# Optimization experiments

Measured on AMD Instinct MI355X. Metric: run time of the kernel, lower is better.

The kernel has to match this reference:

```python
import jax, jax.numpy as jnp
import numpy as np
import math

B, T, C, N = 2, 2048, 1024, 16  # batch, seq, h_dim, n_heads
D = C // N

def setup_inputs() -> dict:
    key = jax.random.key(0)
    k1, k2, k3 = jax.random.split(key, 3)
    x = jax.random.normal(k1, (B, T, C), dtype=jnp.float32)
    Wqkv = jax.random.normal(k2, (C, 3 * C), dtype=jnp.float32) * (1.0 / math.sqrt(C))
    bqkv = jnp.zeros((3 * C,), dtype=jnp.float32)
    Wproj = jax.random.normal(k3, (C, C), dtype=jnp.float32) * (1.0 / math.sqrt(C))
    bproj = jnp.zeros((C,), dtype=jnp.float32)
    return {"x": x, "Wqkv": Wqkv, "bqkv": bqkv, "Wproj": Wproj, "bproj": bproj}

def reference(x, Wqkv, bqkv, Wproj, bproj):
    B_, T_, C_ = x.shape
    N_, D_ = N, C_ // N
    qkv = x @ Wqkv + bqkv                                  # (B,T,3C)
    q, k, v = jnp.split(qkv, 3, axis=-1)
    q = q.reshape(B_, T_, N_, D_).transpose(0, 2, 1, 3)    # (B,N,T,D)
    k = k.reshape(B_, T_, N_, D_).transpose(0, 2, 1, 3)
    v = v.reshape(B_, T_, N_, D_).transpose(0, 2, 1, 3)
    # causal mask: lower-triangular ones, broadcast over (B, 1, T, T)
    mask = jnp.tril(jnp.ones((T_, T_), dtype=jnp.float32))[None, None]
    weights = jnp.einsum('bntd,bnsd->bnts', q, k) / math.sqrt(D_)
    # faithful to original: adds tiny 1e-9 to masked entries (NOT -inf)
    weights = weights + (1.0 - mask) * 1e-9
    normalized = jax.nn.softmax(weights, axis=-1)
    attn = jnp.einsum('bnts,bnsd->bntd', normalized, v)    # (B,N,T,D)
    attn = attn.transpose(0, 2, 1, 3).reshape(B_, T_, N_ * D_)
    out = attn @ Wproj + bproj                              # (B,T,C)
    return out
```

## Files before the change

kernel.cpp:

```cpp
#include <hip/hip_runtime.h>
#include <hip/hip_bf16.h>

#define BB 2
#define TT 2048
#define CC 1024
#define NHEAD 16
#define DHEAD 64
#define MM (BB*TT)
#define KVB 128

using bf16 = __hip_bfloat16;
typedef __bf16 bf16x8 __attribute__((ext_vector_type(8)));
typedef __bf16 bf16x4 __attribute__((ext_vector_type(4)));
typedef float f32x4 __attribute__((ext_vector_type(4)));

static __device__ __forceinline__ bf16 f2b(float f) { return __float2bfloat16(f); }
static __device__ __forceinline__ float fast_exp2(float f) { return __builtin_amdgcn_exp2f(f); }

static __device__ __forceinline__ void gload16(const bf16* g, bf16* l) {
  __builtin_amdgcn_global_load_lds((__attribute__((address_space(1))) const void*)g,
                                   (__attribute__((address_space(3))) void*)l, 16, 0, 0);
}

__global__ __launch_bounds__(256)
void k_prep(const float* __restrict__ x, bf16* __restrict__ Xb,
            const float* __restrict__ Wqkv, bf16* __restrict__ WqkvT,
            const float* __restrict__ Wproj, bf16* __restrict__ WprojT)
{
  int bid = blockIdx.x;
  const int tid = threadIdx.x;
  if (bid < 1024) {
    int base = bid * 1024 + tid;
#pragma unroll
    for (int k = 0; k < 4; ++k) {
      int i = base + k * 256;
      float4 v = reinterpret_cast<const float4*>(x)[i];
      bf16 o[4] = { f2b(v.x), f2b(v.y), f2b(v.z), f2b(v.w) };
      reinterpret_cast<uint2*>(Xb)[i] = *reinterpret_cast<uint2*>(o);
    }
    return;
  }
  bid -= 1024;
  __shared__ float tile[32][33];
  const float* W; bf16* WT; int R, Cc, bx, by;
  if (bid < 3072) {
    W = Wqkv;  WT = WqkvT;  R = CC; Cc = 3*CC;
    bx = bid % 96; by = bid / 96;
  } else {
    bid -= 3072;
    W = Wproj; WT = WprojT; R = CC; Cc = CC;
    bx = bid % 32; by = bid / 32;
  }
  int c0 = bx * 32, r0 = by * 32;
  int tx = tid & 31, ty = tid >> 5;
#pragma unroll
  for (int i = 0; i < 4; ++i)
    tile[ty + 8*i][tx] = W[(size_t)(r0 + ty + 8*i) * Cc + c0 + tx];
  __syncthreads();
#pragma unroll
  for (int i = 0; i < 4; ++i)
    WT[(size_t)(c0 + ty + 8*i) * R + r0 + tx] = f2b(tile[tx][ty + 8*i]);
}

__global__ void k_vtrans(const bf16* __restrict__ V, bf16* __restrict__ VT) {
  __shared__ bf16 tile[32][33];
  const int bn = blockIdx.z;
  const int d0 = blockIdx.x * 32, t0 = blockIdx.y * 32;
  const size_t base = (size_t)bn * TT * DHEAD;
  int tx = threadIdx.x, ty = threadIdx.y;
#pragma unroll
  for (int i = 0; i < 4; ++i)
    tile[ty + 8*i][tx] = V[base + (size_t)(t0 + ty + 8*i) * DHEAD + d0 + tx];
  __syncthreads();
#pragma unroll
  for (int i = 0; i < 4; ++i)
    VT[base + (size_t)(d0 + ty + 8*i) * TT + t0 + tx] = tile[tx][ty + 8*i];
}

#define NTK 32
__global__ __launch_bounds__(512, 2)
void k_gemm_qkv(const bf16* __restrict__ Ag, const bf16* __restrict__ Bg,
                const float* __restrict__ bias,
                bf16* __restrict__ Qb, bf16* __restrict__ Kb, bf16* __restrict__ Vb)
{
  const int tid = threadIdx.x;
  const int w = tid >> 6, l = tid & 63;
  const int l16 = l & 15, l4 = l >> 4;
  const int wr = w >> 2, wc = w & 3;

  const int flat = blockIdx.x;
  const int xcd = flat & 7, local = flat >> 3;
  const int bx = (xcd & 1) * 6 + local % 6;
  const int by = (xcd >> 1) * 8 + local / 6;
  const int m0 = by * 128, n0 = bx * 256;

  __shared__ __align__(16) bf16 sm[36864];

  f32x4 acc[4][4];
#pragma unroll
  for (int m = 0; m < 4; ++m)
#pragma unroll
    for (int n = 0; n < 4; ++n) acc[m][n] = 0.f;

  const int srow = tid >> 2;
  const int scol = ((tid & 3) ^ ((tid >> 3) & 3)) * 8;

#define STAGE(buf, kt) do {                                                            \
    const int kb = (kt) * 32 + scol;                                                   \
    gload16(&Ag[(size_t)(m0 +       srow) * CC + kb], &sm[(buf)*12288        + w*512]);\
    gload16(&Bg[(size_t)(n0 +       srow) * CC + kb], &sm[(buf)*12288 + 4096 + w*512]);\
    gload16(&Bg[(size_t)(n0 + 128 + srow) * CC + kb], &sm[(buf)*12288 + 8192 + w*512]);\
  } while (0)

  STAGE(0, 0);
  STAGE(1, 1);
  STAGE(2, 2);
  asm volatile("s_waitcnt vmcnt(6)" ::: "memory");
  __builtin_amdgcn_s_barrier();

  const int slotA = (l4 ^ ((l16 >> 1) & 3)) * 8;
  const int aoff = wr * 2048 + l16 * 32 + slotA;
  const int boff = 4096 + wc * 2048 + l16 * 32 + slotA;

  int rb = 0;
  for (int kt = 0; kt < NTK; ++kt) {
    const int base = rb * 12288;

    bf16x8 af[4], bfr[4];
#pragma unroll
    for (int m = 0; m < 4; ++m)
      af[m] = *reinterpret_cast<const bf16x8*>(&sm[base + aoff + m*512]);
#pragma unroll
    for (int n = 0; n < 4; ++n)
      bfr[n] = *reinterpret_cast<const bf16x8*>(&sm[base + boff + n*512]);
    __builtin_amdgcn_s_setprio(1);
#pragma unroll
    for (int m = 0; m < 4; ++m)
#pragma unroll
      for (int n = 0; n < 4; ++n)
        acc[m][n] = __builtin_amdgcn_mfma_f32_16x16x32_bf16(af[m], bfr[n], acc[m][n], 0, 0, 0);
    __builtin_amdgcn_s_setprio(0);

    __builtin_amdgcn_s_barrier();
    if (kt + 3 < NTK) {
      STAGE(rb, kt + 3);
      asm volatile("s_waitcnt vmcnt(6)" ::: "memory");
    } else if (kt + 2 < NTK) {
      asm volatile("s_waitcnt vmcnt(3)" ::: "memory");
    } else if (kt + 1 < NTK) {
      asm volatile("s_waitcnt vmcnt(0)" ::: "memory");
    }
    __builtin_amdgcn_s_barrier();
    rb = (rb + 1 == 3) ? 0 : rb + 1;
  }
#undef STAGE

  const int ccol = n0 + wc * 64;
  const int which = ccol >> 10;
  bf16* __restrict__ dst = (which == 0) ? Qb : (which == 1) ? Kb : Vb;
  const float qsc = (which == 0) ? 0.125f * 1.4426950408889634f : 1.0f;
#pragma unroll
  for (int m = 0; m < 4; ++m)
#pragma unroll
    for (int n = 0; n < 4; ++n) {
      int gc = ccol + n*16 + l16;
      float bv = bias[gc];
      int c = gc & (CC-1), head = c >> 6, d = c & 63;
#pragma unroll
      for (int j = 0; j < 4; ++j) {
        int gr = m0 + wr*64 + m*16 + l4*4 + j;
        int b = gr >> 11, t = gr & (TT-1);
        dst[(((size_t)b*NHEAD + head)*TT + t)*DHEAD + d] = f2b((acc[m][n][j] + bv) * qsc);
      }
    }
}

__global__ __launch_bounds__(512, 1)
void k_gemm_proj(const bf16* __restrict__ Ag, const bf16* __restrict__ Bg,
                 const float* __restrict__ bias, float* __restrict__ outF)
{
  const int tid = threadIdx.x;
  const int w = tid >> 6, l = tid & 63;
  const int l16 = l & 15, l4 = l >> 4;
  const int wr = w >> 2, wc = w & 3;

  const int flat = blockIdx.x;
  const int swz = (flat & 7) * 32 + (flat >> 3);
  const int bx = swz >> 5, by = swz & 31;
  const int m0 = by * 128, n0 = bx * 128;

  __shared__ __align__(16) bf16 sm[24576];

  f32x4 acc[4][2];
#pragma unroll
  for (int m = 0; m < 4; ++m)
#pragma unroll
    for (int n = 0; n < 2; ++n) acc[m][n] = 0.f;

  const int srow = tid >> 2;
  const int scol = ((tid & 3) ^ ((tid >> 3) & 3)) * 8;

#define STAGE(buf, kt) do {                                                            \
    const int kb = (kt) * 32 + scol;                                                   \
    gload16(&Ag[(size_t)(m0 + srow) * CC + kb], &sm[(buf)*8192        + w*512]);       \
    gload16(&Bg[(size_t)(n0 + srow) * CC + kb], &sm[(buf)*8192 + 4096 + w*512]);       \
  } while (0)

  STAGE(0, 0);
  STAGE(1, 1);
  STAGE(2, 2);
  asm volatile("s_waitcnt vmcnt(4)" ::: "memory");
  __builtin_amdgcn_s_barrier();

  const int slotA = (l4 ^ ((l16 >> 1) & 3)) * 8;
  const int aoff = wr * 2048 + l16 * 32 + slotA;
  const int boff = 4096 + wc * 1024 + l16 * 32 + slotA;

  int rb = 0;
  for (int kt = 0; kt < NTK; ++kt) {
    const int base = rb * 8192;

    bf16x8 af[4], bfr[2];
#pragma unroll
    for (int m = 0; m < 4; ++m)
      af[m] = *reinterpret_cast<const bf16x8*>(&sm[base + aoff + m*512]);
#pragma unroll
    for (int n = 0; n < 2; ++n)
      bfr[n] = *reinterpret_cast<const bf16x8*>(&sm[base + boff + n*512]);
    __builtin_amdgcn_s_setprio(1);
#pragma unroll
    for (int m = 0; m < 4; ++m)
#pragma unroll
      for (int n = 0; n < 2; ++n)
        acc[m][n] = __builtin_amdgcn_mfma_f32_16x16x32_bf16(af[m], bfr[n], acc[m][n], 0, 0, 0);
    __builtin_amdgcn_s_setprio(0);

    __builtin_amdgcn_s_barrier();
    if (kt + 3 < NTK) {
      STAGE(rb, kt + 3);
      asm volatile("s_waitcnt vmcnt(4)" ::: "memory");
    } else if (kt + 2 < NTK) {
      asm volatile("s_waitcnt vmcnt(2)" ::: "memory");
    } else if (kt + 1 < NTK) {
      asm volatile("s_waitcnt vmcnt(0)" ::: "memory");
    }
    __builtin_amdgcn_s_barrier();
    rb = (rb + 1 == 3) ? 0 : rb + 1;
  }
#undef STAGE

#pragma unroll
  for (int m = 0; m < 4; ++m)
#pragma unroll
    for (int n = 0; n < 2; ++n) {
      int gc = n0 + wc*32 + n*16 + l16;
      float bv = bias[gc];
#pragma unroll
      for (int j = 0; j < 4; ++j) {
        int gr = m0 + wr*64 + m*16 + l4*4 + j;
        outF[(size_t)gr * CC + gc] = acc[m][n][j] + bv;
      }
    }
}

__global__ __launch_bounds__(512, 2)
void k_attn(const bf16* __restrict__ Qg, const bf16* __restrict__ Kg,
            const bf16* __restrict__ VTg, bf16* __restrict__ Aout)
{
  const int tid  = threadIdx.x;
  const int wave = tid >> 6, lane = tid & 63;
  const int l16 = lane & 15, l4 = lane >> 4;

  const int flat = blockIdx.x;
  const int xcd = flat & 7, i6 = flat >> 3;
  const int bn = xcd*4 + (i6 >> 4);
  const int q0 = (i6 & 15) * 128;
  const int b = bn >> 4, h = bn & (NHEAD-1);

  __shared__ __align__(16) bf16 KsF[128*64];
  __shared__ __align__(16) bf16 VtF[64*128];
  __shared__ __align__(16) bf16 PlF[8*16*128];

  const size_t hb = (size_t)bn * TT * DHEAD;
  const bf16* __restrict__ Kbase = Kg + hb;
  const bf16* __restrict__ Vbase = VTg + hb;

  bf16x8 qf[2];
#pragma unroll
  for (int kk = 0; kk < 2; ++kk)
    qf[kk] = *reinterpret_cast<const bf16x8*>(
        &Qg[hb + (size_t)(q0 + wave*16 + l16) * DHEAD + kk*32 + l4*8]);

  f32x4 o[4];
#pragma unroll
  for (int n = 0; n < 4; ++n) o[n] = 0.f;
  float mrun = -1e30f, lrun = 0.f;

  const int krow = tid >> 2, kq = tid & 3;
  const int vrow = tid >> 3, vq = tid & 7;

  bf16x8 kreg[2], vreg[2];
#pragma unroll
  for (int i = 0; i < 2; ++i) {
    kreg[i] = *reinterpret_cast<const bf16x8*>(&Kbase[(size_t)krow * DHEAD + kq*16 + 8*i]);
    vreg[i] = *reinterpret_cast<const bf16x8*>(&Vbase[(size_t)vrow * TT + vq*16 + 8*i]);
  }
#pragma unroll
  for (int i = 0; i < 2; ++i) {
    *reinterpret_cast<bf16x8*>(&KsF[krow*64 + ((kq*2 + i) ^ (krow & 7))*8]) = kreg[i];
    *reinterpret_cast<bf16x8*>(&VtF[vrow*128 + ((vq*2 + i) ^ (vrow & 7))*8]) = vreg[i];
  }

  bf16* PlW = &PlF[wave * 2048];

  for (int t0 = 0; t0 < TT; t0 += KVB) {
    __syncthreads();
    const bool more = (t0 + KVB < TT);
    if (more) {
#pragma unroll
      for (int i = 0; i < 2; ++i) {
        kreg[i] = *reinterpret_cast<const bf16x8*>(
            &Kbase[(size_t)(t0 + KVB + krow) * DHEAD + kq*16 + 8*i]);
        vreg[i] = *reinterpret_cast<const bf16x8*>(
            &Vbase[(size_t)vrow * TT + t0 + KVB + vq*16 + 8*i]);
      }
    }

    f32x4 s[8];
#pragma unroll
    for (int n = 0; n < 8; ++n) s[n] = 0.f;
    __builtin_amdgcn_s_setprio(1);
#pragma unroll
    for (int n = 0; n < 8; ++n) {
      bf16x8 kf0 = *reinterpret_cast<const bf16x8*>(
          &KsF[(n*16 + l16)*64 + ((l4    ) ^ (l16 & 7))*8]);
      bf16x8 kf1 = *reinterpret_cast<const bf16x8*>(
          &KsF[(n*16 + l16)*64 + ((4 + l4) ^ (l16 & 7))*8]);
      s[n] = __builtin_amdgcn_mfma_f32_16x16x32_bf16(kf0, qf[0], s[n], 0, 0, 0);
      s[n] = __builtin_amdgcn_mfma_f32_16x16x32_bf16(kf1, qf[1], s[n], 0, 0, 0);
    }
    __builtin_amdgcn_s_setprio(0);

    float mx[8];
#pragma unroll
    for (int n = 0; n < 8; ++n)
      mx[n] = fmaxf(fmaxf(s[n][0], s[n][1]), fmaxf(s[n][2], s[n][3]));
    float m01 = fmaxf(mx[0], mx[1]), m23 = fmaxf(mx[2], mx[3]);
    float m45 = fmaxf(mx[4], mx[5]), m67 = fmaxf(mx[6], mx[7]);
    float pm = fmaxf(fmaxf(m01, m23), fmaxf(m45, m67));
    pm = fmaxf(pm, __shfl_xor(pm, 16, 64));
    pm = fmaxf(pm, __shfl_xor(pm, 32, 64));

    if (!__all(pm <= mrun + 8.f)) {
      float mn = fmaxf(mrun, pm);
      float corr = fast_exp2(mrun - mn);
      mrun = mn;
      lrun *= corr;
      float cj[4];
#pragma unroll
      for (int j = 0; j < 4; ++j)
        cj[j] = __shfl(corr, ((lane >> 4) << 2) + j, 64);
#pragma unroll
      for (int n = 0; n < 4; ++n)
#pragma unroll
        for (int j = 0; j < 4; ++j) o[n][j] *= cj[j];
    }

    float ps[4] = {0.f, 0.f, 0.f, 0.f};
#pragma unroll
    for (int n = 0; n < 8; ++n) {
      bf16x4 pk;
#pragma unroll
      for (int j = 0; j < 4; ++j) {
        float pv = fast_exp2(s[n][j] - mrun);
        ps[j] += pv;
        pk[j] = (__bf16)pv;
      }
      *reinterpret_cast<bf16x4*>(
          &PlW[l16*128 + ((2*n + (l4 >> 1)) ^ (l16 & 7))*8 + (l4 & 1)*4]) = pk;
    }
    float psum = (ps[0] + ps[1]) + (ps[2] + ps[3]);
    psum += __shfl_xor(psum, 16, 64);
    psum += __shfl_xor(psum, 32, 64);
    lrun += psum;

    bf16x8 pf[4];
#pragma unroll
    for (int kk = 0; kk < 4; ++kk)
      pf[kk] = *reinterpret_cast<const bf16x8*>(
          &PlW[l16*128 + ((4*kk + l4) ^ (l16 & 7))*8]);
    __builtin_amdgcn_s_setprio(1);
#pragma unroll
    for (int n = 0; n < 4; ++n)
#pragma unroll
      for (int kk = 0; kk < 4; ++kk) {
        bf16x8 vf = *reinterpret_cast<const bf16x8*>(
            &VtF[(n*16 + l16)*128 + ((4*kk + l4) ^ (l16 & 7))*8]);
        o[n] = __builtin_amdgcn_mfma_f32_16x16x32_bf16(pf[kk], vf, o[n], 0, 0, 0);
      }
    __builtin_amdgcn_s_setprio(0);

    __syncthreads();
    if (more) {
#pragma unroll
      for (int i = 0; i < 2; ++i) {
        *reinterpret_cast<bf16x8*>(&KsF[krow*64 + ((kq*2 + i) ^ (krow & 7))*8]) = kreg[i];
        *reinterpret_cast<bf16x8*>(&VtF[vrow*128 + ((vq*2 + i) ^ (vrow & 7))*8]) = vreg[i];
      }
    }
  }

  float linv = 1.0f / lrun;
  float lj[4];
#pragma unroll
  for (int j = 0; j < 4; ++j)
    lj[j] = __shfl(linv, ((lane >> 4) << 2) + j, 64);
#pragma unroll
  for (int j = 0; j < 4; ++j) {
    int gt = q0 + wave*16 + l4*4 + j;
#pragma unroll
    for (int n = 0; n < 4; ++n)
      Aout[((size_t)(b*TT + gt))*CC + h*DHEAD + n*16 + l16] = f2b(o[n][j] * lj[j]);
  }
}

extern "C" void kernel_launch(void* const* d_in, const int* in_sizes, int n_in,
                              void* d_out, int out_size, void* d_ws, size_t ws_size,
                              hipStream_t stream)
{
  const float* x     = (const float*)d_in[0];
  const float* Wqkv  = (const float*)d_in[1];
  const float* bqkv  = (const float*)d_in[2];
  const float* Wproj = (const float*)d_in[3];
  const float* bproj = (const float*)d_in[4];
  float* out = (float*)d_out;

  char* p = (char*)d_ws;
  bf16* Xb     = (bf16*)p;  p += (size_t)MM*CC*2;
  bf16* WqkvT  = (bf16*)p;  p += (size_t)3*CC*CC*2;
  bf16* WprojT = (bf16*)p;  p += (size_t)CC*CC*2;
  bf16* Qb     = (bf16*)p;  p += (size_t)MM*CC*2;
  bf16* Kb     = (bf16*)p;  p += (size_t)MM*CC*2;
  bf16* Vb     = (bf16*)p;  p += (size_t)MM*CC*2;
  bf16* Attn   = (bf16*)p;  p += (size_t)MM*CC*2;
  bf16* VTb    = Xb;

  k_prep<<<5120, 256, 0, stream>>>(x, Xb, Wqkv, WqkvT, Wproj, WprojT);
  k_gemm_qkv<<<384, 512, 0, stream>>>(Xb, WqkvT, bqkv, Qb, Kb, Vb);
  k_vtrans<<<dim3(DHEAD/32, TT/32, BB*NHEAD), dim3(32, 8), 0, stream>>>(Vb, VTb);
  k_attn<<<512, 512, 0, stream>>>(Qb, Kb, VTb, Attn);
  k_gemm_proj<<<256, 512, 0, stream>>>(Attn, WprojT, bproj, out);
}
```

Measured before the change: 122.9 us.

## Give each attention wave two query fragments to reuse K/V LDS reads

Cuts the attention block from 8 waves to 4, with each wave now handling 32 query rows as two 16-row fragments. Every K and V fragment read from LDS now feeds two MFMAs, which halves LDS read traffic per FLOP. Each thread also loads twice as much K/V per tile to make up for the fewer threads. The trade is higher register pressure, from doubled S and O accumulators and Q fragments, and fewer waves per block to hide latency.

```diff
diff --git a/kernel.cpp b/kernel.cpp
--- a/kernel.cpp
+++ b/kernel.cpp
@@ -263,7 +263,55 @@
     }
 }
 
-__global__ __launch_bounds__(512, 2)
+static __device__ __forceinline__ void softmax_frag(
+    f32x4 (&s)[8], f32x4 (&o)[4], float &mrun, float &lrun,
+    bf16* __restrict__ PlRow, int lane, int l16, int l4)
+{
+  float mx[8];
+#pragma unroll
+  for (int n = 0; n < 8; ++n)
+    mx[n] = fmaxf(fmaxf(s[n][0], s[n][1]), fmaxf(s[n][2], s[n][3]));
+  float m01 = fmaxf(mx[0], mx[1]), m23 = fmaxf(mx[2], mx[3]);
+  float m45 = fmaxf(mx[4], mx[5]), m67 = fmaxf(mx[6], mx[7]);
+  float pm = fmaxf(fmaxf(m01, m23), fmaxf(m45, m67));
+  pm = fmaxf(pm, __shfl_xor(pm, 16, 64));
+  pm = fmaxf(pm, __shfl_xor(pm, 32, 64));
+
+  if (!__all(pm <= mrun + 8.f)) {
+    float mn = fmaxf(mrun, pm);
+    float corr = fast_exp2(mrun - mn);
+    mrun = mn;
+    lrun *= corr;
+    float cj[4];
+#pragma unroll
+    for (int j = 0; j < 4; ++j)
+      cj[j] = __shfl(corr, ((lane >> 4) << 2) + j, 64);
+#pragma unroll
+    for (int n = 0; n < 4; ++n)
+#pragma unroll
+      for (int j = 0; j < 4; ++j) o[n][j] *= cj[j];
+  }
+
+  float ps[4] = {0.f, 0.f, 0.f, 0.f};
+#pragma unroll
+  for (int n = 0; n < 8; ++n) {
+    bf16x4 pk;
+#pragma unroll
+    for (int j = 0; j < 4; ++j) {
+      float pv = fast_exp2(s[n][j] - mrun);
+      ps[j] += pv;
+      pk[j] = (__bf16)pv;
+    }
+    *reinterpret_cast<bf16x4*>(
+        &PlRow[((2*n + (l4 >> 1)) ^ (l16 & 7))*8 + (l4 & 1)*4]) = pk;
+  }
+  float psum = (ps[0] + ps[1]) + (ps[2] + ps[3]);
+  psum += __shfl_xor(psum, 16, 64);
+  psum += __shfl_xor(psum, 32, 64);
+  lrun += psum;
+}
+
+__global__ __launch_bounds__(256, 2)
 void k_attn(const bf16* __restrict__ Qg, const bf16* __restrict__ Kg,
             const bf16* __restrict__ VTg, bf16* __restrict__ Aout)
 {
@@ -279,56 +327,60 @@
 
   __shared__ __align__(16) bf16 KsF[128*64];
   __shared__ __align__(16) bf16 VtF[64*128];
-  __shared__ __align__(16) bf16 PlF[8*16*128];
+  __shared__ __align__(16) bf16 PlF[4*32*128];
 
   const size_t hb = (size_t)bn * TT * DHEAD;
   const bf16* __restrict__ Kbase = Kg + hb;
   const bf16* __restrict__ Vbase = VTg + hb;
 
-  bf16x8 qf[2];
-#pragma unroll
-  for (int kk = 0; kk < 2; ++kk)
-    qf[kk] = *reinterpret_cast<const bf16x8*>(
-        &Qg[hb + (size_t)(q0 + wave*16 + l16) * DHEAD + kk*32 + l4*8]);
-
-  f32x4 o[4];
-#pragma unroll
-  for (int n = 0; n < 4; ++n) o[n] = 0.f;
-  float mrun = -1e30f, lrun = 0.f;
-
-  const int krow = tid >> 2, kq = tid & 3;
-  const int vrow = tid >> 3, vq = tid & 7;
-
-  bf16x8 kreg[2], vreg[2];
-#pragma unroll
-  for (int i = 0; i < 2; ++i) {
-    kreg[i] = *reinterpret_cast<const bf16x8*>(&Kbase[(size_t)krow * DHEAD + kq*16 + 8*i]);
-    vreg[i] = *reinterpret_cast<const bf16x8*>(&Vbase[(size_t)vrow * TT + vq*16 + 8*i]);
-  }
-#pragma unroll
-  for (int i = 0; i < 2; ++i) {
-    *reinterpret_cast<bf16x8*>(&KsF[krow*64 + ((kq*2 + i) ^ (krow & 7))*8]) = kreg[i];
-    *reinterpret_cast<bf16x8*>(&VtF[vrow*128 + ((vq*2 + i) ^ (vrow & 7))*8]) = vreg[i];
-  }
-
-  bf16* PlW = &PlF[wave * 2048];
+  const int qbase = q0 + wave*32;
+  bf16x8 qf[2][2];
+#pragma unroll
+  for (int f = 0; f < 2; ++f)
+#pragma unroll
+    for (int kk = 0; kk < 2; ++kk)
+      qf[f][kk] = *reinterpret_cast<const bf16x8*>(
+          &Qg[hb + (size_t)(qbase + f*16 + l16) * DHEAD + kk*32 + l4*8]);
+
+  f32x4 o0[4], o1[4];
+#pragma unroll
+  for (int n = 0; n < 4; ++n) { o0[n] = 0.f; o1[n] = 0.f; }
+  float mrun0 = -1e30f, lrun0 = 0.f;
+  float mrun1 = -1e30f, lrun1 = 0.f;
+
+  const int krow = tid >> 1, kq = tid & 1;
+  const int vrow = tid >> 2, vq = tid & 3;
+
+  bf16x8 kreg[4], vreg[4];
+#pragma unroll
+  for (int i = 0; i < 4; ++i) {
+    kreg[i] = *reinterpret_cast<const bf16x8*>(&Kbase[(size_t)krow * DHEAD + kq*32 + 8*i]);
+    vreg[i] = *reinterpret_cast<const bf16x8*>(&Vbase[(size_t)vrow * TT + vq*32 + 8*i]);
+  }
+#pragma unroll
+  for (int i = 0; i < 4; ++i) {
+    *reinterpret_cast<bf16x8*>(&KsF[krow*64 + ((kq*4 + i) ^ (krow & 7))*8]) = kreg[i];
+    *reinterpret_cast<bf16x8*>(&VtF[vrow*128 + ((vq*4 + i) ^ (vrow & 7))*8]) = vreg[i];
+  }
+
+  bf16* PlW = &PlF[wave * 4096];
 
   for (int t0 = 0; t0 < TT; t0 += KVB) {
     __syncthreads();
     const bool more = (t0 + KVB < TT);
     if (more) {
 #pragma unroll
-      for (int i = 0; i < 2; ++i) {
+      for (int i = 0; i < 4; ++i) {
         kreg[i] = *reinterpret_cast<const bf16x8*>(
-            &Kbase[(size_t)(t0 + KVB + krow) * DHEAD + kq*16 + 8*i]);
+            &Kbase[(size_t)(t0 + KVB + krow) * DHEAD + kq*32 + 8*i]);
         vreg[i] = *reinterpret_cast<const bf16x8*>(
-            &Vbase[(size_t)vrow * TT + t0 + KVB + vq*16 + 8*i]);
+            &Vbase[(size_t)vrow * TT + t0 + KVB + vq*32 + 8*i]);
       }
     }
 
-    f32x4 s[8];
-#pragma unroll
-    for (int n = 0; n < 8; ++n) s[n] = 0.f;
+    f32x4 s0[8], s1[8];
+#pragma unroll
+    for (int n = 0; n < 8; ++n) { s0[n] = 0.f; s1[n] = 0.f; }
     __builtin_amdgcn_s_setprio(1);
 #pragma unroll
     for (int n = 0; n < 8; ++n) {
@@ -336,59 +388,24 @@
           &KsF[(n*16 + l16)*64 + ((l4    ) ^ (l16 & 7))*8]);
       bf16x8 kf1 = *reinterpret_cast<const bf16x8*>(
           &KsF[(n*16 + l16)*64 + ((4 + l4) ^ (l16 & 7))*8]);
-      s[n] = __builtin_amdgcn_mfma_f32_16x16x32_bf16(kf0, qf[0], s[n], 0, 0, 0);
-      s[n] = __builtin_amdgcn_mfma_f32_16x16x32_bf16(kf1, qf[1], s[n], 0, 0, 0);
+      s0[n] = __builtin_amdgcn_mfma_f32_16x16x32_bf16(kf0, qf[0][0], s0[n], 0, 0, 0);
+      s0[n] = __builtin_amdgcn_mfma_f32_16x16x32_bf16(kf1, qf[0][1], s0[n], 0, 0, 0);
+      s1[n] = __builtin_amdgcn_mfma_f32_16x16x32_bf16(kf0, qf[1][0], s1[n], 0, 0, 0);
+      s1[n] = __builtin_amdgcn_mfma_f32_16x16x32_bf16(kf1, qf[1][1], s1[n], 0, 0, 0);
     }
     __builtin_amdgcn_s_setprio(0);
 
-    float mx[8];
-#pragma unroll
-    for (int n = 0; n < 8; ++n)
-      mx[n] = fmaxf(fmaxf(s[n][0], s[n][1]), fmaxf(s[n][2], s[n][3]));
-    float m01 = fmaxf(mx[0], mx[1]), m23 = fmaxf(mx[2], mx[3]);
-    float m45 = fmaxf(mx[4], mx[5]), m67 = fmaxf(mx[6], mx[7]);
-    float pm = fmaxf(fmaxf(m01, m23), fmaxf(m45, m67));
-    pm = fmaxf(pm, __shfl_xor(pm, 16, 64));
-    pm = fmaxf(pm, __shfl_xor(pm, 32, 64));
-
-    if (!__all(pm <= mrun + 8.f)) {
-      float mn = fmaxf(mrun, pm);
-      float corr = fast_exp2(mrun - mn);
-      mrun = mn;
-      lrun *= corr;
-      float cj[4];
-#pragma unroll
-      for (int j = 0; j < 4; ++j)
-        cj[j] = __shfl(corr, ((lane >> 4) << 2) + j, 64);
-#pragma unroll
-      for (int n = 0; n < 4; ++n)
-#pragma unroll
-        for (int j = 0; j < 4; ++j) o[n][j] *= cj[j];
-    }
-
-    float ps[4] = {0.f, 0.f, 0.f, 0.f};
-#pragma unroll
-    for (int n = 0; n < 8; ++n) {
-      bf16x4 pk;
-#pragma unroll
-      for (int j = 0; j < 4; ++j) {
-        float pv = fast_exp2(s[n][j] - mrun);
-        ps[j] += pv;
-        pk[j] = (__bf16)pv;
-      }
-      *reinterpret_cast<bf16x4*>(
-          &PlW[l16*128 + ((2*n + (l4 >> 1)) ^ (l16 & 7))*8 + (l4 & 1)*4]) = pk;
-    }
-    float psum = (ps[0] + ps[1]) + (ps[2] + ps[3]);
-    psum += __shfl_xor(psum, 16, 64);
-    psum += __shfl_xor(psum, 32, 64);
-    lrun += psum;
-
-    bf16x8 pf[4];
-#pragma unroll
-    for (int kk = 0; kk < 4; ++kk)
-      pf[kk] = *reinterpret_cast<const bf16x8*>(
-          &PlW[l16*128 + ((4*kk + l4) ^ (l16 & 7))*8]);
+    softmax_frag(s0, o0, mrun0, lrun0, &PlW[(l16     )*128], lane, l16, l4);
+    softmax_frag(s1, o1, mrun1, lrun1, &PlW[(16 + l16)*128], lane, l16, l4);
+
+    bf16x8 pf0[4], pf1[4];
+#pragma unroll
+    for (int kk = 0; kk < 4; ++kk) {
+      pf0[kk] = *reinterpret_cast<const bf16x8*>(
+          &PlW[(l16     )*128 + ((4*kk + l4) ^ (l16 & 7))*8]);
+      pf1[kk] = *reinterpret_cast<const bf16x8*>(
+          &PlW[(16 + l16)*128 + ((4*kk + l4) ^ (l16 & 7))*8]);
+    }
     __builtin_amdgcn_s_setprio(1);
 #pragma unroll
     for (int n = 0; n < 4; ++n)
@@ -396,31 +413,48 @@
       for (int kk = 0; kk < 4; ++kk) {
         bf16x8 vf = *reinterpret_cast<const bf16x8*>(
             &VtF[(n*16 + l16)*128 + ((4*kk + l4) ^ (l16 & 7))*8]);
-        o[n] = __builtin_amdgcn_mfma_f32_16x16x32_bf16(pf[kk], vf, o[n], 0, 0, 0);
+        o0[n] = __builtin_amdgcn_mfma_f32_16x16x32_bf16(pf0[kk], vf, o0[n], 0, 0, 0);
+        o1[n] = __builtin_amdgcn_mfma_f32_16x16x32_bf16(pf1[kk], vf, o1[n], 0, 0, 0);
       }
     __builtin_amdgcn_s_setprio(0);
 
     __syncthreads();
     if (more) {
 #pragma unroll
-      for (int i = 0; i < 2; ++i) {
-        *reinterpret_cast<bf16x8*>(&KsF[krow*64 + ((kq*2 + i) ^ (krow & 7))*8]) = kreg[i];
-        *reinterpret_cast<bf16x8*>(&VtF[vrow*128 + ((vq*2 + i) ^ (vrow & 7))*8]) = vreg[i];
+      for (int i = 0; i < 4; ++i) {
+        *reinterpret_cast<bf16x8*>(&KsF[krow*64 + ((kq*4 + i) ^ (krow & 7))*8]) = kreg[i];
+        *reinterpret_cast<bf16x8*>(&VtF[vrow*128 + ((vq*4 + i) ^ (vrow & 7))*8]) = vreg[i];
       }
     }
   }
 
-  float linv = 1.0f / lrun;
-  float lj[4];
-#pragma unroll
-  for (int j = 0; j < 4; ++j)
-    lj[j] = __shfl(linv, ((lane >> 4) << 2) + j, 64);
-#pragma unroll
-  for (int j = 0; j < 4; ++j) {
-    int gt = q0 + wave*16 + l4*4 + j;
-#pragma unroll
-    for (int n = 0; n < 4; ++n)
-      Aout[((size_t)(b*TT + gt))*CC + h*DHEAD + n*16 + l16] = f2b(o[n][j] * lj[j]);
+  {
+    float linv = 1.0f / lrun0;
+    float lj[4];
+#pragma unroll
+    for (int j = 0; j < 4; ++j)
+      lj[j] = __shfl(linv, ((lane >> 4) << 2) + j, 64);
+#pragma unroll
+    for (int j = 0; j < 4; ++j) {
+      int gt = qbase + l4*4 + j;
+#pragma unroll
+      for (int n = 0; n < 4; ++n)
+        Aout[((size_t)(b*TT + gt))*CC + h*DHEAD + n*16 + l16] = f2b(o0[n][j] * lj[j]);
+    }
+  }
+  {
+    float linv = 1.0f / lrun1;
+    float lj[4];
+#pragma unroll
+    for (int j = 0; j < 4; ++j)
+      lj[j] = __shfl(linv, ((lane >> 4) << 2) + j, 64);
+#pragma unroll
+    for (int j = 0; j < 4; ++j) {
+      int gt = qbase + 16 + l4*4 + j;
+#pragma unroll
+      for (int n = 0; n < 4; ++n)
+        Aout[((size_t)(b*TT + gt))*CC + h*DHEAD + n*16 + l16] = f2b(o1[n][j] * lj[j]);
+    }
   }
 }
 
@@ -448,6 +482,6 @@
   k_prep<<<5120, 256, 0, stream>>>(x, Xb, Wqkv, WqkvT, Wproj, WprojT);
   k_gemm_qkv<<<384, 512, 0, stream>>>(Xb, WqkvT, bqkv, Qb, Kb, Vb);
   k_vtrans<<<dim3(DHEAD/32, TT/32, BB*NHEAD), dim3(32, 8), 0, stream>>>(Vb, VTb);
-  k_attn<<<512, 512, 0, stream>>>(Qb, Kb, VTb, Attn);
+  k_attn<<<512, 256, 0, stream>>>(Qb, Kb, VTb, Attn);
   k_gemm_proj<<<256, 512, 0, stream>>>(Attn, WprojT, bproj, out);
 }
```

New measurement: 124.4 us. About the same (+1.2%).
